# Performance work log

Hardware: AMD Instinct MI355X
Metric: run time of the kernel (lower is better)

Reference implementation:

```python
import jax, jax.numpy as jnp
import numpy as np

D_MODEL = 512
NUM_HEADS = 8
D_HEAD = D_MODEL // NUM_HEADS


def setup_inputs() -> dict:
    key = jax.random.key(0)
    ks = jax.random.split(key, 9)
    B, L = 4, 2048
    s = 1.0 / np.sqrt(D_MODEL)
    inp = {
        "x": jax.random.normal(ks[0], (B, L, D_MODEL), dtype=jnp.float32),
        "Wq": jax.random.uniform(ks[1], (D_MODEL, D_MODEL), jnp.float32, -s, s),
        "bq": jax.random.uniform(ks[2], (D_MODEL,), jnp.float32, -s, s),
        "Wk": jax.random.uniform(ks[3], (D_MODEL, D_MODEL), jnp.float32, -s, s),
        "bk": jax.random.uniform(ks[4], (D_MODEL,), jnp.float32, -s, s),
        "Wv": jax.random.uniform(ks[5], (D_MODEL, D_MODEL), jnp.float32, -s, s),
        "bv": jax.random.uniform(ks[6], (D_MODEL,), jnp.float32, -s, s),
        "Wo": jax.random.uniform(ks[7], (D_MODEL, D_MODEL), jnp.float32, -s, s),
        "bo": jax.random.uniform(ks[8], (D_MODEL,), jnp.float32, -s, s),
    }
    return inp


def reference(x, Wq, bq, Wk, bk, Wv, bv, Wo, bo):
    B, L, _ = x.shape
    def split_heads(t):  # [B,L,D] -> [B,H,L,d]
        return t.reshape(B, L, NUM_HEADS, D_HEAD).transpose(0, 2, 1, 3)
    Q = split_heads(x @ Wq + bq)
    K = split_heads(x @ Wk + bk)
    V = split_heads(x @ Wv + bv)
    scale = 1.0 / jnp.sqrt(jnp.asarray(D_HEAD, dtype=x.dtype))
    scores = jnp.einsum('bhqd,bhkd->bhqk', Q, K) * scale  # [B,H,L,L]
    weights = jax.nn.softmax(scores, axis=-1)
    z = jnp.einsum('bhqk,bhkd->bhqd', weights, V)  # [B,H,L,d]
    z = z.transpose(0, 2, 1, 3).reshape(B, L, D_MODEL)
    return z @ Wo + bo
```

## Files before the change

kernel.cpp:

```cpp
#include <hip/hip_runtime.h>
#include <hip/hip_bf16.h>
#include <math.h>


#define MDIM 8192
#define DMODEL 512
#define NHEAD 8
#define DHEAD 64
#define LSEQ 2048

typedef __attribute__((ext_vector_type(8))) short short8;
typedef __attribute__((ext_vector_type(4))) float floatx4;

struct alignas(16) bf16x8 { __hip_bfloat16 v[8]; };
struct alignas(8)  bf16x4 { __hip_bfloat16 v[4]; };

__device__ __forceinline__ void load_lds16(const __hip_bfloat16* g, __hip_bfloat16* l) {
    __builtin_amdgcn_global_load_lds(
        (const __attribute__((address_space(1))) void*)g,
        (__attribute__((address_space(3))) void*)l,
        16, 0, 0);
}

__device__ __forceinline__ float fast_exp2(float x) {
#if __has_builtin(__builtin_amdgcn_exp2f)
    return __builtin_amdgcn_exp2f(x);
#else
    return __expf(x * 0.69314718055994531f);
#endif
}

__global__ __launch_bounds__(256) void cast_x_kernel(
    const float* __restrict__ x, __hip_bfloat16* __restrict__ xb)
{
    size_t i = ((size_t)blockIdx.x * 256 + threadIdx.x) * 8;
    float4 a = *reinterpret_cast<const float4*>(x + i);
    float4 b = *reinterpret_cast<const float4*>(x + i + 4);
    bf16x8 o;
    o.v[0] = __float2bfloat16(a.x); o.v[1] = __float2bfloat16(a.y);
    o.v[2] = __float2bfloat16(a.z); o.v[3] = __float2bfloat16(a.w);
    o.v[4] = __float2bfloat16(b.x); o.v[5] = __float2bfloat16(b.y);
    o.v[6] = __float2bfloat16(b.z); o.v[7] = __float2bfloat16(b.w);
    *reinterpret_cast<bf16x8*>(xb + i) = o;
}

__global__ __launch_bounds__(256) void transpose_cast_w(
    const float* __restrict__ Wq, const float* __restrict__ Wk,
    const float* __restrict__ Wv, const float* __restrict__ Wo,
    __hip_bfloat16* __restrict__ Wt)
{
    __shared__ float t[32][33];
    const int z = blockIdx.z;
    const float* W = z == 0 ? Wq : (z == 1 ? Wk : (z == 2 ? Wv : Wo));
    __hip_bfloat16* dst = Wt + ((size_t)z << 18);
    int k0 = blockIdx.x * 32, n0 = blockIdx.y * 32;
    int c = threadIdx.x & 31, r = threadIdx.x >> 5;
    #pragma unroll
    for (int i = 0; i < 4; ++i)
        t[r + 8 * i][c] = W[(size_t)(k0 + r + 8 * i) * DMODEL + n0 + c];
    __syncthreads();
    #pragma unroll
    for (int i = 0; i < 4; ++i)
        dst[(size_t)(n0 + r + 8 * i) * DMODEL + k0 + c] = __float2bfloat16(t[c][r + 8 * i]);
}

__global__ __launch_bounds__(256) void gemm_qkv_mfma(
    const __hip_bfloat16* __restrict__ xb,
    const __hip_bfloat16* __restrict__ Wt,
    const float* __restrict__ bq, const float* __restrict__ bk,
    const float* __restrict__ bv,
    __hip_bfloat16* __restrict__ Q2, __hip_bfloat16* __restrict__ K2,
    __hip_bfloat16* __restrict__ V2)
{
    __shared__ __hip_bfloat16 As[128 * 64];
    __shared__ __hip_bfloat16 Bs[128 * 64];

    const int tid = threadIdx.x;
    const int wid = tid >> 6, lane = tid & 63;
    const int l16 = lane & 15, quad = lane >> 4;
    const int wr = wid >> 1, wc = wid & 1;
    const int row0 = blockIdx.x * 128;
    const int which = blockIdx.y >> 2;
    const int col0 = (blockIdx.y & 3) * 128;
    const __hip_bfloat16* Wb = Wt + ((size_t)which << 18);
    const float* bias = which == 0 ? bq : (which == 1 ? bk : bv);

    const int r8 = lane >> 3, slot = lane & 7;
    const int cchunk = slot ^ (r8 & 7);

    floatx4 acc[4][4];
    #pragma unroll
    for (int i = 0; i < 4; ++i)
        #pragma unroll
        for (int j = 0; j < 4; ++j) acc[i][j] = floatx4{0.f, 0.f, 0.f, 0.f};

    for (int kt = 0; kt < DMODEL / 64; ++kt) {
        __syncthreads();
        #pragma unroll
        for (int j = 0; j < 4; ++j) {
            int seg = wid * 4 + j;
            int m = seg * 8 + r8;
            load_lds16(xb + (size_t)(row0 + m) * DMODEL + kt * 64 + cchunk * 8,
                       As + seg * 512);
            load_lds16(Wb + (size_t)(col0 + m) * DMODEL + kt * 64 + cchunk * 8,
                       Bs + seg * 512);
        }
        __syncthreads();

        #pragma unroll
        for (int ks = 0; ks < 2; ++ks) {
            const int c = ks * 4 + quad;
            short8 af[4], bf[4];
            #pragma unroll
            for (int mt = 0; mt < 4; ++mt) {
                int m = wr * 64 + mt * 16 + l16;
                af[mt] = *reinterpret_cast<const short8*>(As + m * 64 + ((c ^ (m & 7)) << 3));
            }
            #pragma unroll
            for (int nt = 0; nt < 4; ++nt) {
                int n = wc * 64 + nt * 16 + l16;
                bf[nt] = *reinterpret_cast<const short8*>(Bs + n * 64 + ((c ^ (n & 7)) << 3));
            }
            if (which < 2) {
                #pragma unroll
                for (int mt = 0; mt < 4; ++mt)
                    #pragma unroll
                    for (int nt = 0; nt < 4; ++nt)
                        acc[mt][nt] = __builtin_amdgcn_mfma_f32_16x16x32_bf16(
                            bf[nt], af[mt], acc[mt][nt], 0, 0, 0);
            } else {
                #pragma unroll
                for (int mt = 0; mt < 4; ++mt)
                    #pragma unroll
                    for (int nt = 0; nt < 4; ++nt)
                        acc[mt][nt] = __builtin_amdgcn_mfma_f32_16x16x32_bf16(
                            af[mt], bf[nt], acc[mt][nt], 0, 0, 0);
            }
        }
    }

    const float QSCALE = 0.18033688011112042f;

    if (which < 2) {
        __hip_bfloat16* dst = (which == 0) ? Q2 : K2;
        #pragma unroll
        for (int mt = 0; mt < 4; ++mt) {
            const int mm = row0 + wr * 64 + mt * 16 + l16;
            const int b = mm >> 11, l = mm & 2047;
            int rowi;
            if (which == 0) {
                rowi = l;
            } else {
                int hi = l & ~127, w7 = l & 127;
                rowi = hi | (w7 & 96) | (((w7 >> 3) & 3) << 2)
                          | (((w7 >> 2) & 1) << 4) | (w7 & 3);
            }
            #pragma unroll
            for (int nt = 0; nt < 4; ++nt) {
                const int nnb = col0 + wc * 64 + nt * 16 + quad * 4;
                const float4 bv4 = *reinterpret_cast<const float4*>(&bias[nnb]);
                const int h = nnb >> 6, d = nnb & 63;
                const int s = d >> 5, q4 = (d >> 3) & 3, jb = d & 7;
                bf16x4 pk;
                if (which == 0) {
                    pk.v[0] = __float2bfloat16((acc[mt][nt][0] + bv4.x) * QSCALE);
                    pk.v[1] = __float2bfloat16((acc[mt][nt][1] + bv4.y) * QSCALE);
                    pk.v[2] = __float2bfloat16((acc[mt][nt][2] + bv4.z) * QSCALE);
                    pk.v[3] = __float2bfloat16((acc[mt][nt][3] + bv4.w) * QSCALE);
                } else {
                    pk.v[0] = __float2bfloat16(acc[mt][nt][0] + bv4.x);
                    pk.v[1] = __float2bfloat16(acc[mt][nt][1] + bv4.y);
                    pk.v[2] = __float2bfloat16(acc[mt][nt][2] + bv4.z);
                    pk.v[3] = __float2bfloat16(acc[mt][nt][3] + bv4.w);
                }
                size_t idx = ((((size_t)(b * NHEAD + h) * 128 + (rowi >> 4)) * 2 + s) << 9)
                             + q4 * 128 + (rowi & 15) * 8 + jb;
                *reinterpret_cast<bf16x4*>(dst + idx) = pk;
            }
        }
    } else {
        #pragma unroll
        for (int mt = 0; mt < 4; ++mt) {
            const int mmb = row0 + wr * 64 + mt * 16 + quad * 4;
            const int b = mmb >> 11, lb = mmb & 2047;
            #pragma unroll
            for (int nt = 0; nt < 4; ++nt) {
                const int nn = col0 + wc * 64 + nt * 16 + l16;
                const int h = nn >> 6, d = nn & 63;
                const float bv = bias[nn];
                bf16x4 pk;
                #pragma unroll
                for (int r = 0; r < 4; ++r)
                    pk.v[r] = __float2bfloat16(acc[mt][nt][r] + bv);
                size_t idx = ((((size_t)(b * NHEAD + h) * 64 + (lb >> 5)) * 4 + (d >> 4)) << 9)
                             + ((lb >> 3) & 3) * 128 + (d & 15) * 8 + (lb & 7);
                *reinterpret_cast<bf16x4*>(V2 + idx) = pk;
            }
        }
    }
}

__global__ __launch_bounds__(256) void gemm_out_mfma(
    const __hip_bfloat16* __restrict__ Zb,
    const __hip_bfloat16* __restrict__ WoT,
    const float* __restrict__ bo, float* __restrict__ out)
{
    __shared__ __hip_bfloat16 As[128 * 64];
    __shared__ __hip_bfloat16 Bs[128 * 64];

    const int tid = threadIdx.x;
    const int wid = tid >> 6, lane = tid & 63;
    const int l16 = lane & 15, quad = lane >> 4;
    const int wr = wid >> 1, wc = wid & 1;
    const int row0 = blockIdx.x * 128;
    const int col0 = blockIdx.y * 128;
    const int r8 = lane >> 3, slot = lane & 7;
    const int cchunk = slot ^ (r8 & 7);

    floatx4 acc[4][4];
    #pragma unroll
    for (int i = 0; i < 4; ++i)
        #pragma unroll
        for (int j = 0; j < 4; ++j) acc[i][j] = floatx4{0.f, 0.f, 0.f, 0.f};

    for (int kt = 0; kt < DMODEL / 64; ++kt) {
        __syncthreads();
        #pragma unroll
        for (int j = 0; j < 4; ++j) {
            int seg = wid * 4 + j;
            int m = seg * 8 + r8;
            load_lds16(Zb + (size_t)(row0 + m) * DMODEL + kt * 64 + cchunk * 8,
                       As + seg * 512);
            load_lds16(WoT + (size_t)(col0 + m) * DMODEL + kt * 64 + cchunk * 8,
                       Bs + seg * 512);
        }
        __syncthreads();

        #pragma unroll
        for (int ks = 0; ks < 2; ++ks) {
            const int c = ks * 4 + quad;
            short8 af[4], bf[4];
            #pragma unroll
            for (int mt = 0; mt < 4; ++mt) {
                int m = wr * 64 + mt * 16 + l16;
                af[mt] = *reinterpret_cast<const short8*>(As + m * 64 + ((c ^ (m & 7)) << 3));
            }
            #pragma unroll
            for (int nt = 0; nt < 4; ++nt) {
                int n = wc * 64 + nt * 16 + l16;
                bf[nt] = *reinterpret_cast<const short8*>(Bs + n * 64 + ((c ^ (n & 7)) << 3));
            }
            #pragma unroll
            for (int mt = 0; mt < 4; ++mt)
                #pragma unroll
                for (int nt = 0; nt < 4; ++nt)
                    acc[mt][nt] = __builtin_amdgcn_mfma_f32_16x16x32_bf16(
                        af[mt], bf[nt], acc[mt][nt], 0, 0, 0);
        }
    }

    #pragma unroll
    for (int mt = 0; mt < 4; ++mt) {
        const int mmbase = row0 + wr * 64 + mt * 16 + quad * 4;
        #pragma unroll
        for (int nt = 0; nt < 4; ++nt) {
            const int nn = col0 + wc * 64 + nt * 16 + l16;
            const float bias_v = bo[nn];
            #pragma unroll
            for (int r = 0; r < 4; ++r)
                out[(size_t)(mmbase + r) * DMODEL + nn] = acc[mt][nt][r] + bias_v;
        }
    }
}

__global__ __launch_bounds__(256) void attn_mfma(
    const __hip_bfloat16* __restrict__ Q2,
    const __hip_bfloat16* __restrict__ K2,
    const __hip_bfloat16* __restrict__ V2,
    __hip_bfloat16* __restrict__ Z)
{
    __shared__ float smem[4608];
    float* Lred = smem;
    float* Ored = smem + 256;

    const int bh = blockIdx.x & 31;
    const int qt = blockIdx.x >> 5;
    const int q0 = qt * 64;
    const int tid = threadIdx.x;
    const int wid = tid >> 6, lane = tid & 63;
    const int l16 = lane & 15, quad = lane >> 4;

    const __hip_bfloat16* Kc = K2 + (((size_t)bh * 128 * 2) << 9);
    const __hip_bfloat16* Vc = V2 + (((size_t)bh * 64 * 4) << 9);

    short8 qb[4][2];
    #pragma unroll
    for (int nt = 0; nt < 4; ++nt)
        #pragma unroll
        for (int s = 0; s < 2; ++s)
            qb[nt][s] = *reinterpret_cast<const short8*>(
                Q2 + ((((size_t)bh * 128 + qt * 4 + nt) * 2 + s) << 9) + lane * 8);

    floatx4 acc[4][4];
    #pragma unroll
    for (int i = 0; i < 4; ++i)
        #pragma unroll
        for (int j = 0; j < 4; ++j) acc[i][j] = floatx4{0.f, 0.f, 0.f, 0.f};
    float lsum[4] = {0.f, 0.f, 0.f, 0.f};

    for (int kt = 0; kt < LSEQ / 128; ++kt) {
        short8 kb[2][2], vb[4];
        #pragma unroll
        for (int t = 0; t < 2; ++t)
            #pragma unroll
            for (int s = 0; s < 2; ++s)
                kb[t][s] = *reinterpret_cast<const short8*>(
                    Kc + ((((size_t)(kt * 8 + wid * 2 + t)) * 2 + s) << 9) + lane * 8);
        #pragma unroll
        for (int dt = 0; dt < 4; ++dt)
            vb[dt] = *reinterpret_cast<const short8*>(
                Vc + ((((size_t)(kt * 4 + wid)) * 4 + dt) << 9) + lane * 8);

        floatx4 sacc[2][4];
        #pragma unroll
        for (int t = 0; t < 2; ++t)
            #pragma unroll
            for (int nt = 0; nt < 4; ++nt) sacc[t][nt] = floatx4{0.f, 0.f, 0.f, 0.f};
        #pragma unroll
        for (int s = 0; s < 2; ++s) {
            #pragma unroll
            for (int nt = 0; nt < 4; ++nt) {
                sacc[0][nt] = __builtin_amdgcn_mfma_f32_16x16x32_bf16(
                    kb[0][s], qb[nt][s], sacc[0][nt], 0, 0, 0);
                sacc[1][nt] = __builtin_amdgcn_mfma_f32_16x16x32_bf16(
                    kb[1][s], qb[nt][s], sacc[1][nt], 0, 0, 0);
            }
        }

        short8 pa[4];
        #pragma unroll
        for (int nt = 0; nt < 4; ++nt) {
            union { short8 s8; __hip_bfloat16 h[8]; } u;
            #pragma unroll
            for (int t = 0; t < 2; ++t)
                #pragma unroll
                for (int r = 0; r < 4; ++r) {
                    float p = fast_exp2(sacc[t][nt][r]);
                    lsum[nt] += p;
                    u.h[t * 4 + r] = __float2bfloat16(p);
                }
            pa[nt] = u.s8;
        }

        #pragma unroll
        for (int dt = 0; dt < 4; ++dt)
            #pragma unroll
            for (int nt = 0; nt < 4; ++nt)
                acc[nt][dt] = __builtin_amdgcn_mfma_f32_16x16x32_bf16(
                    pa[nt], vb[dt], acc[nt][dt], 0, 0, 0);
    }

    #pragma unroll
    for (int nt = 0; nt < 4; ++nt) {
        float v = lsum[nt];
        v += __shfl_xor(v, 16);
        v += __shfl_xor(v, 32);
        lsum[nt] = v;
    }
    if (quad == 0) {
        #pragma unroll
        for (int nt = 0; nt < 4; ++nt)
            Lred[wid * 64 + nt * 16 + l16] = lsum[nt];
    }

    const int b = bh >> 3, h = bh & 7;
    const int ql = tid >> 2;
    const int dg = tid & 3;
    float inv = 0.f;

    for (int dt = 0; dt < 4; ++dt) {
        __syncthreads();
        #pragma unroll
        for (int nt = 0; nt < 4; ++nt)
            *reinterpret_cast<floatx4*>(
                &Ored[(wid * 16 + l16) * 68 + nt * 16 + quad * 4]) = acc[nt][dt];
        __syncthreads();

        if (dt == 0)
            inv = 1.f / (Lred[ql] + Lred[64 + ql] + Lred[128 + ql] + Lred[192 + ql]);

        bf16x4 zo;
        #pragma unroll
        for (int i = 0; i < 4; ++i) {
            int d = dg * 4 + i;
            float ssum = Ored[d * 68 + ql] + Ored[(16 + d) * 68 + ql]
                       + Ored[(32 + d) * 68 + ql] + Ored[(48 + d) * 68 + ql];
            zo.v[i] = __float2bfloat16(ssum * inv);
        }
        *reinterpret_cast<bf16x4*>(
            Z + (size_t)(b * LSEQ + q0 + ql) * DMODEL + h * 64 + dt * 16 + dg * 4) = zo;
    }
}

extern "C" void kernel_launch(void* const* d_in, const int* in_sizes, int n_in,
                              void* d_out, int out_size, void* d_ws, size_t ws_size,
                              hipStream_t stream)
{
    const float* x  = (const float*)d_in[0];
    const float* Wq = (const float*)d_in[1]; const float* bq = (const float*)d_in[2];
    const float* Wk = (const float*)d_in[3]; const float* bk = (const float*)d_in[4];
    const float* Wv = (const float*)d_in[5]; const float* bv = (const float*)d_in[6];
    const float* Wo = (const float*)d_in[7]; const float* bo = (const float*)d_in[8];
    float* out = (float*)d_out;

    const size_t nqkv = (size_t)MDIM * DMODEL;
    __hip_bfloat16* xb = (__hip_bfloat16*)d_ws;
    __hip_bfloat16* Wt = xb + nqkv;
    __hip_bfloat16* Q2 = Wt + ((size_t)4 << 18);
    __hip_bfloat16* K2 = Q2 + nqkv;
    __hip_bfloat16* V2 = K2 + nqkv;
    __hip_bfloat16* Zb = V2 + nqkv;

    cast_x_kernel<<<dim3(MDIM * DMODEL / (256 * 8)), 256, 0, stream>>>(x, xb);
    transpose_cast_w<<<dim3(16, 16, 4), 256, 0, stream>>>(Wq, Wk, Wv, Wo, Wt);

    gemm_qkv_mfma<<<dim3(MDIM / 128, 12), 256, 0, stream>>>(
        xb, Wt, bq, bk, bv, Q2, K2, V2);

    attn_mfma<<<dim3(32 * (LSEQ / 64)), 256, 0, stream>>>(Q2, K2, V2, Zb);

    gemm_out_mfma<<<dim3(MDIM / 128, DMODEL / 128), 256, 0, stream>>>(
        Zb, Wt + ((size_t)3 << 18), bo, out);
}
```

Baseline: 162.2 us.

## Use cheap round-half-up bf16 packing and halve output GEMM tile width

Replaces the RNE __float2bfloat16 conversions with a cheaper pack that adds 0x8000 and permutes the high halves into a packed pair. It is used in the cast, QKV epilogue, attention softmax P packing and Z output, with the softmax packing in the hot loop. The output projection GEMM tile shrinks from 128x128 to 128x64, doubling the grid from 256 to 512 blocks for better CU occupancy at the cost of more A-tile reloads. The rounding drops round-to-nearest-even tie handling and NaN handling, which slightly changes numerics.

```diff
diff --git a/kernel.cpp b/kernel.cpp
--- a/kernel.cpp
+++ b/kernel.cpp
@@ -30,18 +30,24 @@
 #endif
 }
 
+__device__ __forceinline__ unsigned pack2bf16(float a, float b) {
+    unsigned ua = __builtin_bit_cast(unsigned, a) + 0x8000u;
+    unsigned ub = __builtin_bit_cast(unsigned, b) + 0x8000u;
+    return __builtin_amdgcn_perm(ub, ua, 0x07060302u);
+}
+
 __global__ __launch_bounds__(256) void cast_x_kernel(
     const float* __restrict__ x, __hip_bfloat16* __restrict__ xb)
 {
     size_t i = ((size_t)blockIdx.x * 256 + threadIdx.x) * 8;
     float4 a = *reinterpret_cast<const float4*>(x + i);
     float4 b = *reinterpret_cast<const float4*>(x + i + 4);
-    bf16x8 o;
-    o.v[0] = __float2bfloat16(a.x); o.v[1] = __float2bfloat16(a.y);
-    o.v[2] = __float2bfloat16(a.z); o.v[3] = __float2bfloat16(a.w);
-    o.v[4] = __float2bfloat16(b.x); o.v[5] = __float2bfloat16(b.y);
-    o.v[6] = __float2bfloat16(b.z); o.v[7] = __float2bfloat16(b.w);
-    *reinterpret_cast<bf16x8*>(xb + i) = o;
+    union { bf16x8 o; uint4 u; } o;
+    o.u.x = pack2bf16(a.x, a.y);
+    o.u.y = pack2bf16(a.z, a.w);
+    o.u.z = pack2bf16(b.x, b.y);
+    o.u.w = pack2bf16(b.z, b.w);
+    *reinterpret_cast<bf16x8*>(xb + i) = o.o;
 }
 
 __global__ __launch_bounds__(256) void transpose_cast_w(
@@ -143,6 +149,7 @@
 
     if (which < 2) {
         __hip_bfloat16* dst = (which == 0) ? Q2 : K2;
+        const float sc = (which == 0) ? QSCALE : 1.0f;
         #pragma unroll
         for (int mt = 0; mt < 4; ++mt) {
             const int mm = row0 + wr * 64 + mt * 16 + l16;
@@ -161,21 +168,14 @@
                 const float4 bv4 = *reinterpret_cast<const float4*>(&bias[nnb]);
                 const int h = nnb >> 6, d = nnb & 63;
                 const int s = d >> 5, q4 = (d >> 3) & 3, jb = d & 7;
-                bf16x4 pk;
-                if (which == 0) {
-                    pk.v[0] = __float2bfloat16((acc[mt][nt][0] + bv4.x) * QSCALE);
-                    pk.v[1] = __float2bfloat16((acc[mt][nt][1] + bv4.y) * QSCALE);
-                    pk.v[2] = __float2bfloat16((acc[mt][nt][2] + bv4.z) * QSCALE);
-                    pk.v[3] = __float2bfloat16((acc[mt][nt][3] + bv4.w) * QSCALE);
-                } else {
-                    pk.v[0] = __float2bfloat16(acc[mt][nt][0] + bv4.x);
-                    pk.v[1] = __float2bfloat16(acc[mt][nt][1] + bv4.y);
-                    pk.v[2] = __float2bfloat16(acc[mt][nt][2] + bv4.z);
-                    pk.v[3] = __float2bfloat16(acc[mt][nt][3] + bv4.w);
-                }
+                union { bf16x4 b4; uint2 u; } pk;
+                pk.u.x = pack2bf16((acc[mt][nt][0] + bv4.x) * sc,
+                                   (acc[mt][nt][1] + bv4.y) * sc);
+                pk.u.y = pack2bf16((acc[mt][nt][2] + bv4.z) * sc,
+                                   (acc[mt][nt][3] + bv4.w) * sc);
                 size_t idx = ((((size_t)(b * NHEAD + h) * 128 + (rowi >> 4)) * 2 + s) << 9)
                              + q4 * 128 + (rowi & 15) * 8 + jb;
-                *reinterpret_cast<bf16x4*>(dst + idx) = pk;
+                *reinterpret_cast<bf16x4*>(dst + idx) = pk.b4;
             }
         }
     } else {
@@ -188,13 +188,12 @@
                 const int nn = col0 + wc * 64 + nt * 16 + l16;
                 const int h = nn >> 6, d = nn & 63;
                 const float bv = bias[nn];
-                bf16x4 pk;
-                #pragma unroll
-                for (int r = 0; r < 4; ++r)
-                    pk.v[r] = __float2bfloat16(acc[mt][nt][r] + bv);
+                union { bf16x4 b4; uint2 u; } pk;
+                pk.u.x = pack2bf16(acc[mt][nt][0] + bv, acc[mt][nt][1] + bv);
+                pk.u.y = pack2bf16(acc[mt][nt][2] + bv, acc[mt][nt][3] + bv);
                 size_t idx = ((((size_t)(b * NHEAD + h) * 64 + (lb >> 5)) * 4 + (d >> 4)) << 9)
                              + ((lb >> 3) & 3) * 128 + (d & 15) * 8 + (lb & 7);
-                *reinterpret_cast<bf16x4*>(V2 + idx) = pk;
+                *reinterpret_cast<bf16x4*>(V2 + idx) = pk.b4;
             }
         }
     }
@@ -206,20 +205,19 @@
     const float* __restrict__ bo, float* __restrict__ out)
 {
     __shared__ __hip_bfloat16 As[128 * 64];
-    __shared__ __hip_bfloat16 Bs[128 * 64];
+    __shared__ __hip_bfloat16 Bs[64 * 64];
 
     const int tid = threadIdx.x;
     const int wid = tid >> 6, lane = tid & 63;
     const int l16 = lane & 15, quad = lane >> 4;
-    const int wr = wid >> 1, wc = wid & 1;
     const int row0 = blockIdx.x * 128;
-    const int col0 = blockIdx.y * 128;
+    const int col0 = blockIdx.y * 64;
     const int r8 = lane >> 3, slot = lane & 7;
     const int cchunk = slot ^ (r8 & 7);
 
-    floatx4 acc[4][4];
-    #pragma unroll
-    for (int i = 0; i < 4; ++i)
+    floatx4 acc[2][4];
+    #pragma unroll
+    for (int i = 0; i < 2; ++i)
         #pragma unroll
         for (int j = 0; j < 4; ++j) acc[i][j] = floatx4{0.f, 0.f, 0.f, 0.f};
 
@@ -231,7 +229,12 @@
             int m = seg * 8 + r8;
             load_lds16(Zb + (size_t)(row0 + m) * DMODEL + kt * 64 + cchunk * 8,
                        As + seg * 512);
-            load_lds16(WoT + (size_t)(col0 + m) * DMODEL + kt * 64 + cchunk * 8,
+        }
+        #pragma unroll
+        for (int j = 0; j < 2; ++j) {
+            int seg = wid * 2 + j;
+            int n = seg * 8 + r8;
+            load_lds16(WoT + (size_t)(col0 + n) * DMODEL + kt * 64 + cchunk * 8,
                        Bs + seg * 512);
         }
         __syncthreads();
@@ -239,19 +242,19 @@
         #pragma unroll
         for (int ks = 0; ks < 2; ++ks) {
             const int c = ks * 4 + quad;
-            short8 af[4], bf[4];
-            #pragma unroll
-            for (int mt = 0; mt < 4; ++mt) {
-                int m = wr * 64 + mt * 16 + l16;
+            short8 af[2], bf[4];
+            #pragma unroll
+            for (int mt = 0; mt < 2; ++mt) {
+                int m = wid * 32 + mt * 16 + l16;
                 af[mt] = *reinterpret_cast<const short8*>(As + m * 64 + ((c ^ (m & 7)) << 3));
             }
             #pragma unroll
             for (int nt = 0; nt < 4; ++nt) {
-                int n = wc * 64 + nt * 16 + l16;
+                int n = nt * 16 + l16;
                 bf[nt] = *reinterpret_cast<const short8*>(Bs + n * 64 + ((c ^ (n & 7)) << 3));
             }
             #pragma unroll
-            for (int mt = 0; mt < 4; ++mt)
+            for (int mt = 0; mt < 2; ++mt)
                 #pragma unroll
                 for (int nt = 0; nt < 4; ++nt)
                     acc[mt][nt] = __builtin_amdgcn_mfma_f32_16x16x32_bf16(
@@ -260,11 +263,11 @@
     }
 
     #pragma unroll
-    for (int mt = 0; mt < 4; ++mt) {
-        const int mmbase = row0 + wr * 64 + mt * 16 + quad * 4;
+    for (int mt = 0; mt < 2; ++mt) {
+        const int mmbase = row0 + wid * 32 + mt * 16 + quad * 4;
         #pragma unroll
         for (int nt = 0; nt < 4; ++nt) {
-            const int nn = col0 + wc * 64 + nt * 16 + l16;
+            const int nn = col0 + nt * 16 + l16;
             const float bias_v = bo[nn];
             #pragma unroll
             for (int r = 0; r < 4; ++r)
@@ -340,15 +343,20 @@
         short8 pa[4];
         #pragma unroll
         for (int nt = 0; nt < 4; ++nt) {
-            union { short8 s8; __hip_bfloat16 h[8]; } u;
+            float p[8];
             #pragma unroll
             for (int t = 0; t < 2; ++t)
                 #pragma unroll
                 for (int r = 0; r < 4; ++r) {
-                    float p = fast_exp2(sacc[t][nt][r]);
-                    lsum[nt] += p;
-                    u.h[t * 4 + r] = __float2bfloat16(p);
+                    float e = fast_exp2(sacc[t][nt][r]);
+                    lsum[nt] += e;
+                    p[t * 4 + r] = e;
                 }
+            union { short8 s8; unsigned u[4]; } u;
+            u.u[0] = pack2bf16(p[0], p[1]);
+            u.u[1] = pack2bf16(p[2], p[3]);
+            u.u[2] = pack2bf16(p[4], p[5]);
+            u.u[3] = pack2bf16(p[6], p[7]);
             pa[nt] = u.s8;
         }
 
@@ -389,16 +397,19 @@
         if (dt == 0)
             inv = 1.f / (Lred[ql] + Lred[64 + ql] + Lred[128 + ql] + Lred[192 + ql]);
 
-        bf16x4 zo;
+        float zz[4];
         #pragma unroll
         for (int i = 0; i < 4; ++i) {
             int d = dg * 4 + i;
             float ssum = Ored[d * 68 + ql] + Ored[(16 + d) * 68 + ql]
                        + Ored[(32 + d) * 68 + ql] + Ored[(48 + d) * 68 + ql];
-            zo.v[i] = __float2bfloat16(ssum * inv);
-        }
+            zz[i] = ssum * inv;
+        }
+        union { bf16x4 b4; uint2 u; } zo;
+        zo.u.x = pack2bf16(zz[0], zz[1]);
+        zo.u.y = pack2bf16(zz[2], zz[3]);
         *reinterpret_cast<bf16x4*>(
-            Z + (size_t)(b * LSEQ + q0 + ql) * DMODEL + h * 64 + dt * 16 + dg * 4) = zo;
+            Z + (size_t)(b * LSEQ + q0 + ql) * DMODEL + h * 64 + dt * 16 + dg * 4) = zo.b4;
     }
 }
 
@@ -429,6 +440,6 @@
 
     attn_mfma<<<dim3(32 * (LSEQ / 64)), 256, 0, stream>>>(Q2, K2, V2, Zb);
 
-    gemm_out_mfma<<<dim3(MDIM / 128, DMODEL / 128), 256, 0, stream>>>(
+    gemm_out_mfma<<<dim3(MDIM / 128, DMODEL / 64), 256, 0, stream>>>(
         Zb, Wt + ((size_t)3 << 18), bo, out);
 }
```

Measured after the change: 162.0 us. No clear change (-0.1%).

## Prefetch K/V in attention loop, shrink output GEMM tile, tidy epilogues

Applied to the files above, without the earlier changes.

The attention kernel now loads the next K/V tile into registers while computing on the current one, so global load latency can overlap with MFMA and exp work. The exp/row-sum code is split so the sum becomes a tree over eight values. The output GEMM tile shrinks from 128x128 to 128x64, doubling the grid to give more blocks for the 256 CUs. The QKV epilogue branch is merged using a scale variable. Register prefetching raises register pressure in attention, and the wrapped index makes the last iteration do one redundant load.

```diff
diff --git a/kernel.cpp b/kernel.cpp
--- a/kernel.cpp
+++ b/kernel.cpp
@@ -143,6 +143,7 @@
 
     if (which < 2) {
         __hip_bfloat16* dst = (which == 0) ? Q2 : K2;
+        const float sc = (which == 0) ? QSCALE : 1.0f;
         #pragma unroll
         for (int mt = 0; mt < 4; ++mt) {
             const int mm = row0 + wr * 64 + mt * 16 + l16;
@@ -162,17 +163,10 @@
                 const int h = nnb >> 6, d = nnb & 63;
                 const int s = d >> 5, q4 = (d >> 3) & 3, jb = d & 7;
                 bf16x4 pk;
-                if (which == 0) {
-                    pk.v[0] = __float2bfloat16((acc[mt][nt][0] + bv4.x) * QSCALE);
-                    pk.v[1] = __float2bfloat16((acc[mt][nt][1] + bv4.y) * QSCALE);
-                    pk.v[2] = __float2bfloat16((acc[mt][nt][2] + bv4.z) * QSCALE);
-                    pk.v[3] = __float2bfloat16((acc[mt][nt][3] + bv4.w) * QSCALE);
-                } else {
-                    pk.v[0] = __float2bfloat16(acc[mt][nt][0] + bv4.x);
-                    pk.v[1] = __float2bfloat16(acc[mt][nt][1] + bv4.y);
-                    pk.v[2] = __float2bfloat16(acc[mt][nt][2] + bv4.z);
-                    pk.v[3] = __float2bfloat16(acc[mt][nt][3] + bv4.w);
-                }
+                pk.v[0] = __float2bfloat16((acc[mt][nt][0] + bv4.x) * sc);
+                pk.v[1] = __float2bfloat16((acc[mt][nt][1] + bv4.y) * sc);
+                pk.v[2] = __float2bfloat16((acc[mt][nt][2] + bv4.z) * sc);
+                pk.v[3] = __float2bfloat16((acc[mt][nt][3] + bv4.w) * sc);
                 size_t idx = ((((size_t)(b * NHEAD + h) * 128 + (rowi >> 4)) * 2 + s) << 9)
                              + q4 * 128 + (rowi & 15) * 8 + jb;
                 *reinterpret_cast<bf16x4*>(dst + idx) = pk;
@@ -189,9 +183,10 @@
                 const int h = nn >> 6, d = nn & 63;
                 const float bv = bias[nn];
                 bf16x4 pk;
-                #pragma unroll
-                for (int r = 0; r < 4; ++r)
-                    pk.v[r] = __float2bfloat16(acc[mt][nt][r] + bv);
+                pk.v[0] = __float2bfloat16(acc[mt][nt][0] + bv);
+                pk.v[1] = __float2bfloat16(acc[mt][nt][1] + bv);
+                pk.v[2] = __float2bfloat16(acc[mt][nt][2] + bv);
+                pk.v[3] = __float2bfloat16(acc[mt][nt][3] + bv);
                 size_t idx = ((((size_t)(b * NHEAD + h) * 64 + (lb >> 5)) * 4 + (d >> 4)) << 9)
                              + ((lb >> 3) & 3) * 128 + (d & 15) * 8 + (lb & 7);
                 *reinterpret_cast<bf16x4*>(V2 + idx) = pk;
@@ -206,20 +201,19 @@
     const float* __restrict__ bo, float* __restrict__ out)
 {
     __shared__ __hip_bfloat16 As[128 * 64];
-    __shared__ __hip_bfloat16 Bs[128 * 64];
+    __shared__ __hip_bfloat16 Bs[64 * 64];
 
     const int tid = threadIdx.x;
     const int wid = tid >> 6, lane = tid & 63;
     const int l16 = lane & 15, quad = lane >> 4;
-    const int wr = wid >> 1, wc = wid & 1;
     const int row0 = blockIdx.x * 128;
-    const int col0 = blockIdx.y * 128;
+    const int col0 = blockIdx.y * 64;
     const int r8 = lane >> 3, slot = lane & 7;
     const int cchunk = slot ^ (r8 & 7);
 
-    floatx4 acc[4][4];
-    #pragma unroll
-    for (int i = 0; i < 4; ++i)
+    floatx4 acc[2][4];
+    #pragma unroll
+    for (int i = 0; i < 2; ++i)
         #pragma unroll
         for (int j = 0; j < 4; ++j) acc[i][j] = floatx4{0.f, 0.f, 0.f, 0.f};
 
@@ -231,7 +225,12 @@
             int m = seg * 8 + r8;
             load_lds16(Zb + (size_t)(row0 + m) * DMODEL + kt * 64 + cchunk * 8,
                        As + seg * 512);
-            load_lds16(WoT + (size_t)(col0 + m) * DMODEL + kt * 64 + cchunk * 8,
+        }
+        #pragma unroll
+        for (int j = 0; j < 2; ++j) {
+            int seg = wid * 2 + j;
+            int n = seg * 8 + r8;
+            load_lds16(WoT + (size_t)(col0 + n) * DMODEL + kt * 64 + cchunk * 8,
                        Bs + seg * 512);
         }
         __syncthreads();
@@ -239,19 +238,19 @@
         #pragma unroll
         for (int ks = 0; ks < 2; ++ks) {
             const int c = ks * 4 + quad;
-            short8 af[4], bf[4];
-            #pragma unroll
-            for (int mt = 0; mt < 4; ++mt) {
-                int m = wr * 64 + mt * 16 + l16;
+            short8 af[2], bf[4];
+            #pragma unroll
+            for (int mt = 0; mt < 2; ++mt) {
+                int m = wid * 32 + mt * 16 + l16;
                 af[mt] = *reinterpret_cast<const short8*>(As + m * 64 + ((c ^ (m & 7)) << 3));
             }
             #pragma unroll
             for (int nt = 0; nt < 4; ++nt) {
-                int n = wc * 64 + nt * 16 + l16;
+                int n = nt * 16 + l16;
                 bf[nt] = *reinterpret_cast<const short8*>(Bs + n * 64 + ((c ^ (n & 7)) << 3));
             }
             #pragma unroll
-            for (int mt = 0; mt < 4; ++mt)
+            for (int mt = 0; mt < 2; ++mt)
                 #pragma unroll
                 for (int nt = 0; nt < 4; ++nt)
                     acc[mt][nt] = __builtin_amdgcn_mfma_f32_16x16x32_bf16(
@@ -260,11 +259,11 @@
     }
 
     #pragma unroll
-    for (int mt = 0; mt < 4; ++mt) {
-        const int mmbase = row0 + wr * 64 + mt * 16 + quad * 4;
+    for (int mt = 0; mt < 2; ++mt) {
+        const int mmbase = row0 + wid * 32 + mt * 16 + quad * 4;
         #pragma unroll
         for (int nt = 0; nt < 4; ++nt) {
-            const int nn = col0 + wc * 64 + nt * 16 + l16;
+            const int nn = col0 + nt * 16 + l16;
             const float bias_v = bo[nn];
             #pragma unroll
             for (int r = 0; r < 4; ++r)
@@ -308,18 +307,31 @@
         for (int j = 0; j < 4; ++j) acc[i][j] = floatx4{0.f, 0.f, 0.f, 0.f};
     float lsum[4] = {0.f, 0.f, 0.f, 0.f};
 
+    short8 kb[2][2], vb[4];
+    #pragma unroll
+    for (int t = 0; t < 2; ++t)
+        #pragma unroll
+        for (int s = 0; s < 2; ++s)
+            kb[t][s] = *reinterpret_cast<const short8*>(
+                Kc + ((((size_t)(wid * 2 + t)) * 2 + s) << 9) + lane * 8);
+    #pragma unroll
+    for (int dt = 0; dt < 4; ++dt)
+        vb[dt] = *reinterpret_cast<const short8*>(
+            Vc + ((((size_t)wid) * 4 + dt) << 9) + lane * 8);
+
     for (int kt = 0; kt < LSEQ / 128; ++kt) {
-        short8 kb[2][2], vb[4];
+        const int ktn = (kt + 1) & (LSEQ / 128 - 1);
+        short8 nkb[2][2], nvb[4];
         #pragma unroll
         for (int t = 0; t < 2; ++t)
             #pragma unroll
             for (int s = 0; s < 2; ++s)
-                kb[t][s] = *reinterpret_cast<const short8*>(
-                    Kc + ((((size_t)(kt * 8 + wid * 2 + t)) * 2 + s) << 9) + lane * 8);
+                nkb[t][s] = *reinterpret_cast<const short8*>(
+                    Kc + ((((size_t)(ktn * 8 + wid * 2 + t)) * 2 + s) << 9) + lane * 8);
         #pragma unroll
         for (int dt = 0; dt < 4; ++dt)
-            vb[dt] = *reinterpret_cast<const short8*>(
-                Vc + ((((size_t)(kt * 4 + wid)) * 4 + dt) << 9) + lane * 8);
+            nvb[dt] = *reinterpret_cast<const short8*>(
+                Vc + ((((size_t)(ktn * 4 + wid)) * 4 + dt) << 9) + lane * 8);
 
         floatx4 sacc[2][4];
         #pragma unroll
@@ -340,15 +352,16 @@
         short8 pa[4];
         #pragma unroll
         for (int nt = 0; nt < 4; ++nt) {
-            union { short8 s8; __hip_bfloat16 h[8]; } u;
+            float e[8];
             #pragma unroll
             for (int t = 0; t < 2; ++t)
                 #pragma unroll
-                for (int r = 0; r < 4; ++r) {
-                    float p = fast_exp2(sacc[t][nt][r]);
-                    lsum[nt] += p;
-                    u.h[t * 4 + r] = __float2bfloat16(p);
-                }
+                for (int r = 0; r < 4; ++r)
+                    e[t * 4 + r] = fast_exp2(sacc[t][nt][r]);
+            union { short8 s8; __hip_bfloat16 h[8]; } u;
+            #pragma unroll
+            for (int i = 0; i < 8; ++i) u.h[i] = __float2bfloat16(e[i]);
+            lsum[nt] += ((e[0] + e[1]) + (e[2] + e[3])) + ((e[4] + e[5]) + (e[6] + e[7]));
             pa[nt] = u.s8;
         }
 
@@ -358,6 +371,13 @@
             for (int nt = 0; nt < 4; ++nt)
                 acc[nt][dt] = __builtin_amdgcn_mfma_f32_16x16x32_bf16(
                     pa[nt], vb[dt], acc[nt][dt], 0, 0, 0);
+
+        #pragma unroll
+        for (int t = 0; t < 2; ++t)
+            #pragma unroll
+            for (int s = 0; s < 2; ++s) kb[t][s] = nkb[t][s];
+        #pragma unroll
+        for (int dt = 0; dt < 4; ++dt) vb[dt] = nvb[dt];
     }
 
     #pragma unroll
@@ -429,6 +449,6 @@
 
     attn_mfma<<<dim3(32 * (LSEQ / 64)), 256, 0, stream>>>(Q2, K2, V2, Zb);
 
-    gemm_out_mfma<<<dim3(MDIM / 128, DMODEL / 128), 256, 0, stream>>>(
+    gemm_out_mfma<<<dim3(MDIM / 128, DMODEL / 64), 256, 0, stream>>>(
         Zb, Wt + ((size_t)3 << 18), bo, out);
 }
```

Measured after the change: 159.6 us. About the same (-1.6%).
